# Optimization experiments

Measured on AMD Instinct MI355X. Metric: run time of the kernel, lower is better.

The kernel has to match this reference:

```python
import jax, jax.numpy as jnp
import numpy as np

N_ANCHORS = 262144
N_GT = 100
IMG = 1024.0
N_SAMPLE = 256
POS_RATIO = 0.5
POS_T = 0.7
NEG_T = 0.3
ALLOWED_BORDER = 0.0
NUM_FG = int(POS_RATIO * N_SAMPLE)  # 128


def compute_overlap(a, g):
    """IoU between anchors a:(N,4) and gt g:(R,4), py-faster-rcnn +1 pixel convention."""
    area_a = (a[:, 2] - a[:, 0] + 1.0) * (a[:, 3] - a[:, 1] + 1.0)          # (N,)
    area_g = (g[:, 2] - g[:, 0] + 1.0) * (g[:, 3] - g[:, 1] + 1.0)          # (R,)
    iw = jnp.minimum(a[:, None, 2], g[None, :, 2]) - jnp.maximum(a[:, None, 0], g[None, :, 0]) + 1.0
    ih = jnp.minimum(a[:, None, 3], g[None, :, 3]) - jnp.maximum(a[:, None, 1], g[None, :, 1]) + 1.0
    inter = jnp.maximum(iw, 0.0) * jnp.maximum(ih, 0.0)                     # (N,R)
    return inter / (area_a[:, None] + area_g[None, :] - inter)


def bbox_transform(gt, an):
    """Encode gt boxes relative to anchors -> (dx,dy,dw,dh), shape (N,4)."""
    aw = an[:, 2] - an[:, 0] + 1.0
    ah = an[:, 3] - an[:, 1] + 1.0
    acx = an[:, 0] + 0.5 * aw
    acy = an[:, 1] + 0.5 * ah
    gw = gt[:, 2] - gt[:, 0] + 1.0
    gh = gt[:, 3] - gt[:, 1] + 1.0
    gcx = gt[:, 0] + 0.5 * gw
    gcy = gt[:, 1] + 0.5 * gh
    return jnp.stack([(gcx - acx) / aw, (gcy - acy) / ah,
                      jnp.log(gw / aw), jnp.log(gh / ah)], axis=1)


def keep_at_most(mask, k, key):
    """Keep at most k True entries of mask, chosen uniformly at random (fixed shape)."""
    r = jnp.where(mask, jax.random.uniform(key, mask.shape), jnp.inf)
    rank = jnp.argsort(jnp.argsort(r))  # rank[i] = position of i in ascending sort
    return mask & (rank < k)


def anchor_target(anchors, image_shape, gt, key):
    # anchors: (N,4), gt: (R,4)
    R = gt.shape[0]
    inside = ((anchors[:, 0] >= -ALLOWED_BORDER) & (anchors[:, 1] >= -ALLOWED_BORDER)
              & (anchors[:, 2] < ALLOWED_BORDER + image_shape[1])
              & (anchors[:, 3] < ALLOWED_BORDER + image_shape[0]))            # (N,)
    iou = compute_overlap(anchors, gt)                                        # (N,R)
    iou_m = jnp.where(inside[:, None], iou, -1.0)  # restrict to inside anchors
    max_ov = jnp.max(iou_m, axis=1)                                           # (N,)

    k1, k2, k3 = jax.random.split(key, 3)
    labels = jnp.full(anchors.shape[:1], -1.0, dtype=jnp.float32)
    # clobber_positives=False: background first
    labels = jnp.where(inside & (max_ov < NEG_T), 0.0, labels)
    # per-gt argmax anchors (tie set), randomly truncated to at most R like tf.random_shuffle[:R]
    gt_max = jnp.max(iou_m, axis=0)                                           # (R,)
    cand = jnp.any(iou_m == gt_max[None, :], axis=1) & inside                 # (N,)
    cand = keep_at_most(cand, R, k1)
    labels = jnp.where(cand, 1.0, labels)
    labels = jnp.where(inside & (max_ov >= POS_T), 1.0, labels)

    # balance: subsample positives to NUM_FG
    fg = labels == 1.0
    labels = jnp.where(fg & ~keep_at_most(fg, NUM_FG, k2), -1.0, labels)
    # subsample negatives to n_sample - n_fg
    n_fg = jnp.sum(labels == 1.0)
    bg = labels == 0.0
    labels = jnp.where(bg & ~keep_at_most(bg, N_SAMPLE - n_fg, k3), -1.0, labels)
    # umap: outside anchors stay -1
    labels = jnp.where(inside, labels, -1.0)

    # bbox targets: faithful to original tf.gather(gt, to_int32(max_overlaps))
    idx = jnp.clip(max_ov.astype(jnp.int32), 0, R - 1)
    tgt = bbox_transform(gt[idx], anchors)                                    # (N,4)
    tgt = jnp.where(inside[:, None], tgt, 0.0)  # scatter_nd at inside indices
    return labels[None], tgt[None]


def setup_inputs() -> dict:
    key = jax.random.key(0)
    k1, k2, k3, k4 = jax.random.split(key, 4)
    ctr = jax.random.uniform(k1, (N_ANCHORS, 2), minval=-64.0, maxval=IMG + 64.0)
    wh = jax.random.uniform(k2, (N_ANCHORS, 2), minval=16.0, maxval=256.0)
    anchors = jnp.concatenate([ctr - 0.5 * wh, ctr + 0.5 * wh], axis=1)
    gctr = jax.random.uniform(k3, (N_GT, 2), minval=100.0, maxval=IMG - 100.0)
    gwh = jax.random.uniform(k4, (N_GT, 2), minval=30.0, maxval=200.0)
    gt = jnp.concatenate([gctr - 0.5 * gwh, gctr + 0.5 * gwh], axis=1)
    return {"total_anchors": anchors[None],
            "image_shape": jnp.array([IMG, IMG], jnp.float32),
            "gt_boxes": gt[None]}


def reference(total_anchors, image_shape, gt_boxes):
    key = jax.random.key(42)  # original uses unseeded tf.random_shuffle
    labels, bbox_reg_targets = anchor_target(total_anchors[0], image_shape,
                                             gt_boxes[0][:, :4], key)
    return labels, bbox_reg_targets
```

## Files before the change

### kernel.cpp

```cpp
#include <hip/hip_runtime.h>
#include <stdint.h>

#define NGT_MAX 128
#define CAND_CAP 8192
#define CSEL_CAP 512
#define FILT_CAP 16384
#define SUB_CAP 2048


__host__ __device__ inline void tf2x32(uint32_t k0, uint32_t k1, uint32_t c0, uint32_t c1,
                                       uint32_t& o0, uint32_t& o1) {
  uint32_t ks[3] = {k0, k1, k0 ^ k1 ^ 0x1BD11BDAu};
  uint32_t x0 = c0 + ks[0];
  uint32_t x1 = c1 + ks[1];
  const int rot[2][4] = {{13, 15, 26, 6}, {17, 29, 16, 24}};
#pragma unroll
  for (int i = 0; i < 5; ++i) {
#pragma unroll
    for (int j = 0; j < 4; ++j) {
      x0 += x1;
      int r = rot[i & 1][j];
      x1 = (x1 << r) | (x1 >> (32 - r));
      x1 ^= x0;
    }
    x0 += ks[(i + 1) % 3];
    x1 += ks[(i + 2) % 3] + (uint32_t)(i + 1);
  }
  o0 = x0; o1 = x1;
}

__device__ inline uint64_t sel_key(uint32_t i, uint32_t ka, uint32_t kb) {
  uint32_t o0, o1;
  tf2x32(ka, kb, 0u, i, o0, o1);
  uint32_t bits = o0 ^ o1;
  return ((uint64_t)(bits >> 9) << 32) | (uint64_t)i;
}

__device__ inline uint32_t fmap(float v) {
  uint32_t u = __float_as_uint(v);
  return (u & 0x80000000u) ? ~u : (u | 0x80000000u);
}
__device__ inline float funmap(uint32_t m) {
  return (m & 0x80000000u) ? __uint_as_float(m & 0x7FFFFFFFu) : __uint_as_float(~m);
}

__device__ inline void cons_meta(uint32_t baseF, uint32_t baseB, uint32_t* needF,
                                 uint32_t* Tf, uint32_t* needB, uint32_t* Tb) {
  *needF = (baseF > 128u) ? 1u : 0u;
  uint64_t tf = 0, tb = 0;
  if (*needF) {
    tf = (((uint64_t)(128u * 32u)) << 23) / (uint64_t)baseF;
    if (tf > (1u << 23)) tf = (1u << 23);
  }
  uint32_t nfgmin = baseF < 128u ? baseF : 128u;
  uint32_t kbgmax = 256u - nfgmin;
  *needB = (baseB > 8192u + kbgmax) ? 1u : 0u;
  if (*needB) {
    tb = (((uint64_t)(kbgmax * 32u)) << 23) / (uint64_t)(baseB - 8192u);
    if (tb > (1u << 23)) tb = (1u << 23);
  }
  *Tf = (uint32_t)tf;
  *Tb = (uint32_t)tb;
}

__device__ __forceinline__ float iou_ref(const float4& a, float area_a, const float4& gb,
                                         float area_g) {
#pragma clang fp contract(off)
  float iw = fminf(a.z, gb.z) - fmaxf(a.x, gb.x) + 1.0f;
  float ih = fminf(a.w, gb.w) - fmaxf(a.y, gb.y) + 1.0f;
  float inter = fmaxf(iw, 0.0f) * fmaxf(ih, 0.0f);
  return inter / (area_a + area_g - inter);
}

__device__ __forceinline__ float4 tgt_ref(const float4& a, const float4& gb) {
#pragma clang fp contract(off)
  float aw = a.z - a.x + 1.0f;
  float ah = a.w - a.y + 1.0f;
  float acx = a.x + 0.5f * aw;
  float acy = a.y + 0.5f * ah;
  float gw = gb.z - gb.x + 1.0f;
  float gh = gb.w - gb.y + 1.0f;
  float gcx = gb.x + 0.5f * gw;
  float gcy = gb.y + 0.5f * gh;
  return make_float4((gcx - acx) / aw, (gcy - acy) / ah, logf(gw / aw), logf(gh / ah));
}

__global__ void __launch_bounds__(256)
k_main(const float4* __restrict__ anc, const float* __restrict__ img,
       const float4* __restrict__ gt, int N, int R,
       uint32_t* __restrict__ pmax, uint32_t* __restrict__ gmaxu,
       float* __restrict__ LBL, float4* __restrict__ TGT,
       uint32_t* __restrict__ pmeta, uint32_t* __restrict__ counters) {
  __shared__ float4 sgt[NGT_MAX];
  __shared__ float sarea[NGT_MAX];
  __shared__ float sq[16 * 101];
  __shared__ uint32_t scnt[2];
  const int t = threadIdx.x, b = blockIdx.x;
  if (b == 0 && t < 16) counters[t] = 0u;
  if (t < 2) scnt[t] = 0u;
  if (t < R) {
    float4 g = gt[t];
    sgt[t] = g;
    {
#pragma clang fp contract(off)
      sarea[t] = (g.z - g.x + 1.0f) * (g.w - g.y + 1.0f);
    }
  }
  for (int j = t; j < 16 * 101; j += 256) sq[j] = -1.0f;
  __syncthreads();
  const int lane = t & 63, wid = t >> 6;
  const int h = lane >> 5;
  const int al = lane & 31;
  const int p = lane & 3;
  const int i = b * 128 + wid * 32 + al;
  const int gbase = 50 * h;
  const int Rh = R - gbase;
  const float H = img[0], W = img[1];
  float4 a = anc[i];
  bool inside = (a.x >= 0.0f) && (a.y >= 0.0f) && (a.z < W) && (a.w < H);
  float area_a;
  {
#pragma clang fp contract(off)
    area_a = (a.z - a.x + 1.0f) * (a.w - a.y + 1.0f);
  }
  if (!inside) area_a = __uint_as_float(0x7FC00000u);
  const bool b1 = (p == 1), b2 = (p == 2), b3 = (p == 3);
  float part[13];
  float vmax = -1.0f;
#pragma unroll
  for (int s = 0; s < 13; ++s) {
    float v2q[4];
#pragma unroll
    for (int k = 0; k < 4; ++k) {
      const int j = 4 * s + k;
      if (j < 50 && j < Rh) {
        const int g = gbase + j;
        float4 gb = sgt[g];
        float v = iou_ref(a, area_a, gb, sarea[g]);
        vmax = fmaxf(vmax, v);
        int d1 = __builtin_amdgcn_mov_dpp(__float_as_int(v), 0xB1, 0xF, 0xF, true);
        float v1 = fmaxf(v, __int_as_float(d1));
        int d2 = __builtin_amdgcn_mov_dpp(__float_as_int(v1), 0x4E, 0xF, 0xF, true);
        v2q[k] = fmaxf(v1, __int_as_float(d2));
      } else {
        v2q[k] = -1.0f;
      }
    }
    float pp = v2q[0];
    pp = b1 ? v2q[1] : pp;
    pp = b2 ? v2q[2] : pp;
    pp = b3 ? v2q[3] : pp;
    part[s] = pp;
  }
  vmax = fmaxf(vmax, __shfl_xor(vmax, 32));
  float lbl = -1.0f;
  if (inside) {
    if (vmax < 0.3f) lbl = 0.0f;
    if (vmax >= 0.7f) lbl = 1.0f;
  }
  unsigned long long bf = __ballot(lbl == 1.0f) & 0xFFFFFFFFull;
  unsigned long long bb = __ballot(lbl == 0.0f) & 0xFFFFFFFFull;
  if (lane == 0) {
    atomicAdd(&scnt[0], (uint32_t)__popcll(bf));
    atomicAdd(&scnt[1], (uint32_t)__popcll(bb));
  }
  if (h == 0) {
    LBL[i] = lbl;
    float4 o = make_float4(0.f, 0.f, 0.f, 0.f);
    if (inside) {
      int idx = (int)vmax;
      idx = idx < 0 ? 0 : (idx > R - 1 ? R - 1 : idx);
      o = tgt_ref(a, sgt[idx]);
    }
    TGT[i] = o;
  }
#pragma unroll
  for (int s = 0; s < 13; ++s) {
    float v = part[s];
    int x = __builtin_amdgcn_mov_dpp(__float_as_int(v), 0x114, 0xF, 0xF, true);
    v = fmaxf(v, __int_as_float(x));
    x = __builtin_amdgcn_mov_dpp(__float_as_int(v), 0x118, 0xF, 0xF, true);
    v = fmaxf(v, __int_as_float(x));
    part[s] = v;
  }
  const int r = t >> 4;
  if ((t & 15) >= 12) {
#pragma unroll
    for (int s = 0; s < 13; ++s) {
      const int j = 4 * s + p;
      if (j < 50 && j < Rh) sq[r * 101 + gbase + j] = part[s];
    }
  }
  __syncthreads();
  if (t < R) {
    float m = -1.0f;
#pragma unroll 8
    for (int r2 = 0; r2 < 16; ++r2) m = fmaxf(m, sq[r2 * 101 + t]);
    uint32_t u = fmap(m);
    pmax[b * R + t] = u;
    if (u > gmaxu[t]) atomicMax(&gmaxu[t], u);
  }
  if (t == 0) pmeta[b] = scnt[0] | (scnt[1] << 16);
}

__global__ void __launch_bounds__(256)
k_gather(const float4* __restrict__ anc, const float* __restrict__ img,
         const float4* __restrict__ gt, int N, int NBm, int R,
         const uint32_t* __restrict__ pmax, const uint32_t* __restrict__ gmaxu,
         const uint32_t* __restrict__ pmeta,
         float* __restrict__ LBL,
         uint64_t* __restrict__ candList, uint32_t* __restrict__ candLbl,
         uint64_t* __restrict__ listF, uint64_t* __restrict__ listB,
         uint32_t* __restrict__ counters,
         uint32_t k1a, uint32_t k1b, uint32_t k2a, uint32_t k2b,
         uint32_t k3a, uint32_t k3b) {
  __shared__ uint64_t red[256];
  __shared__ int tg[NGT_MAX];
  __shared__ float tgm[NGT_MAX];
  __shared__ uint64_t cbuf[256];
  __shared__ uint32_t cbufL[256];
  __shared__ uint64_t bufF[256], bufB[256];
  __shared__ uint32_t cC, cF, cB, oC, oF, oB;
  __shared__ int tcnt;
  const int t = threadIdx.x, b = blockIdx.x;
  if (t == 0) { tcnt = 0; cC = 0u; cF = 0u; cB = 0u; }
  uint64_t sm = 0;
  for (int j = t; j < NBm; j += 256) {
    uint32_t v = pmeta[j];
    sm += (uint64_t)(v & 0xFFFFu) | ((uint64_t)(v >> 16) << 32);
  }
  red[t] = sm;
  __syncthreads();
  for (int s = 128; s > 0; s >>= 1) {
    if (t < s) red[t] += red[t + s];
    __syncthreads();
  }
  const uint32_t baseF = (uint32_t)(red[0] & 0xFFFFFFFFu);
  const uint32_t baseB = (uint32_t)(red[0] >> 32);
  uint32_t needF, Tf, needB, Tb;
  cons_meta(baseF, baseB, &needF, &Tf, &needB, &Tb);
  if (t < R) {
    uint32_t gm = gmaxu[t];
    uint32_t pm0 = pmax[(2 * b) * R + t];
    uint32_t pm1 = pmax[(2 * b + 1) * R + t];
    if (pm0 == gm || pm1 == gm) {
      int pp = atomicAdd(&tcnt, 1);
      tg[pp] = t;
      tgm[pp] = funmap(gm);
    }
  }
  __syncthreads();
  const int C0 = tcnt;
  const int i = b * 256 + t;
  float old = LBL[i];
  bool isc = false;
  if (C0 > 0) {
    const float H = img[0], W = img[1];
    float4 a = anc[i];
    bool inside = (a.x >= 0.0f) && (a.y >= 0.0f) && (a.z < W) && (a.w < H);
    if (inside) {
      float area_a;
      {
#pragma clang fp contract(off)
        area_a = (a.z - a.x + 1.0f) * (a.w - a.y + 1.0f);
      }
      for (int j = 0; j < C0; ++j) {
        float4 gb = gt[tg[j]];
        float ag;
        {
#pragma clang fp contract(off)
          ag = (gb.z - gb.x + 1.0f) * (gb.w - gb.y + 1.0f);
        }
        float v = iou_ref(a, area_a, gb, ag);
        isc = isc || (v == tgm[j]);
      }
    }
  }
  if (isc) {
    uint32_t code = (old == 1.0f) ? 2u : ((old == 0.0f) ? 1u : 0u);
    uint32_t pp = atomicAdd(&cC, 1u);
    cbuf[pp] = sel_key((uint32_t)i, k1a, k1b);
    cbufL[pp] = code;
  }
  float l1 = isc ? 1.0f : old;
  float out = l1;
  if (l1 == 1.0f) {
    uint64_t key = sel_key((uint32_t)i, k2a, k2b);
    if (needF && (uint32_t)(key >> 32) >= Tf) {
      out = -1.0f;
    } else {
      uint32_t pp = atomicAdd(&cF, 1u);
      bufF[pp] = key;
    }
  } else if (l1 == 0.0f) {
    uint64_t key = sel_key((uint32_t)i, k3a, k3b);
    if (needB && (uint32_t)(key >> 32) >= Tb) {
      out = -1.0f;
    } else {
      uint32_t pp = atomicAdd(&cB, 1u);
      bufB[pp] = key;
    }
  }
  LBL[i] = out;
  __syncthreads();
  if (t == 0 && cC) oC = atomicAdd(&counters[0], cC);
  if (t == 64 && cF) oF = atomicAdd(&counters[4], cF);
  if (t == 128 && cB) oB = atomicAdd(&counters[5], cB);
  __syncthreads();
  for (uint32_t j = t; j < cC; j += 256) {
    uint32_t pp = oC + j;
    if (pp < CAND_CAP) { candList[pp] = cbuf[j]; candLbl[pp] = cbufL[j]; }
  }
  for (uint32_t j = t; j < cF; j += 256) {
    uint32_t pp = oF + j;
    if (pp < FILT_CAP) listF[pp] = bufF[j];
  }
  for (uint32_t j = t; j < cB; j += 256) {
    uint32_t pp = oB + j;
    if (pp < FILT_CAP) listB[pp] = bufB[j];
  }
}

__device__ __forceinline__ void do_select(const uint64_t* list, uint32_t Mf, uint32_t k,
                                          uint32_t T, float* LBL, uint32_t* h,
                                          uint32_t* c0, uint32_t* c1, uint64_t* sub,
                                          uint32_t* scal, const uint32_t* drop,
                                          uint32_t nd) {
  const int t = threadIdx.x;
  if (Mf <= k) return;
  int bl = (T > 1u) ? (32 - __clz(T - 1u)) : 0;
  int shift = bl > 8 ? bl - 8 : 0;
  h[t] = 0u;
  if (t == 0) { scal[0] = 0u; scal[1] = 0u; scal[2] = 0u; }
  __syncthreads();
  for (uint32_t j = t; j < Mf; j += 256) {
    uint64_t key = list[j];
    bool skip = false;
    for (uint32_t d = 0; d < nd; ++d) skip = skip || (drop[d] == (uint32_t)key);
    if (!skip) atomicAdd(&h[((uint32_t)(key >> 32)) >> shift], 1u);
  }
  __syncthreads();
  c0[t] = h[t];
  __syncthreads();
  uint32_t* s = c0;
  uint32_t* d2 = c1;
  for (int dd = 1; dd < 256; dd <<= 1) {
    uint32_t v = s[t];
    if (t >= dd) v += s[t - dd];
    d2[t] = v;
    __syncthreads();
    uint32_t* tmp = s; s = d2; d2 = tmp;
  }
  uint32_t inc = s[t];
  uint32_t exc = inc - h[t];
  if (exc < k && inc >= k) { scal[1] = (uint32_t)t; scal[2] = k - exc; }
  __syncthreads();
  const uint32_t binb = scal[1], rneed = scal[2];
  for (uint32_t j = t; j < Mf; j += 256) {
    uint64_t key = list[j];
    bool skip = false;
    for (uint32_t d = 0; d < nd; ++d) skip = skip || (drop[d] == (uint32_t)key);
    if (skip) continue;
    uint32_t bin = ((uint32_t)(key >> 32)) >> shift;
    if (bin > binb) {
      LBL[(uint32_t)key] = -1.0f;
    } else if (bin == binb) {
      uint32_t pp = atomicAdd(&scal[0], 1u);
      if (pp < SUB_CAP) sub[pp] = key;
    }
  }
  __syncthreads();
  uint32_t c = scal[0] < SUB_CAP ? scal[0] : SUB_CAP;
  for (uint32_t s2 = t; s2 < c; s2 += 256) {
    uint64_t key = sub[s2];
    uint32_t rank = 0u;
    for (uint32_t j = 0; j < c; ++j) rank += (sub[j] < key) ? 1u : 0u;
    if (rank >= rneed) LBL[(uint32_t)key] = -1.0f;
  }
  __syncthreads();
}

__global__ void __launch_bounds__(256)
k_sel(float* __restrict__ LBL, uint64_t* __restrict__ listF,
      uint64_t* __restrict__ listB, const uint64_t* __restrict__ candList,
      const uint32_t* __restrict__ candLbl, const uint32_t* __restrict__ pmeta,
      uint32_t* __restrict__ counters, int NBm, int R,
      uint32_t k3a, uint32_t k3b) {
  __shared__ uint64_t red[256];
  __shared__ uint64_t ck[CSEL_CAP];
  __shared__ uint32_t cc[CSEL_CAP];
  __shared__ uint32_t drop[256];
  __shared__ uint32_t h[256], c0s[256], c1s[256];
  __shared__ uint64_t sub[SUB_CAP];
  __shared__ uint32_t scal[8];
  const int t = threadIdx.x;
  uint64_t sm = 0;
  for (int j = t; j < NBm; j += 256) {
    uint32_t v = pmeta[j];
    sm += (uint64_t)(v & 0xFFFFu) | ((uint64_t)(v >> 16) << 32);
  }
  red[t] = sm;
  if (t < 8) scal[t] = 0u;
  uint32_t C = counters[0];
  if (C > CSEL_CAP) C = CSEL_CAP;
  for (uint32_t s = t; s < C; s += 256) { ck[s] = candList[s]; cc[s] = candLbl[s]; }
  __syncthreads();
  for (int s = 128; s > 0; s >>= 1) {
    if (t < s) red[t] += red[t + s];
    __syncthreads();
  }
  const uint32_t baseF = (uint32_t)(red[0] & 0xFFFFFFFFu);
  const uint32_t baseB = (uint32_t)(red[0] >> 32);
  uint32_t needFc, TfC, needBc, TbC;
  cons_meta(baseF, baseB, &needFc, &TfC, &needBc, &TbC);
  const uint32_t MfB0 = counters[5] < FILT_CAP ? counters[5] : FILT_CAP;
  for (uint32_t e = t; e < C; e += 256) {
    uint64_t key = ck[e];
    bool keep = true;
    if (C > (uint32_t)R) {
      uint32_t rank = 0;
      for (uint32_t j = 0; j < C; ++j) rank += (ck[j] < key) ? 1u : 0u;
      keep = (rank < (uint32_t)R);
    }
    uint32_t code = cc[e];
    uint32_t idx = (uint32_t)key;
    if (keep) {
      if (code != 2u) atomicAdd(&scal[4], 1u);
      if (code == 1u) atomicAdd(&scal[5], 1u);
    } else if (code != 2u) {
      uint32_t pp = atomicAdd(&scal[3], 1u);
      if (pp < 256) drop[pp] = idx;
      if (code == 0u) {
        LBL[idx] = -1.0f;
      } else {
        uint64_t key3 = sel_key(idx, k3a, k3b);
        if (needBc && (uint32_t)(key3 >> 32) >= TbC) {
          LBL[idx] = -1.0f;
        } else {
          uint32_t qq = atomicAdd(&scal[6], 1u);
          if (MfB0 + qq < FILT_CAP) listB[MfB0 + qq] = key3;
          LBL[idx] = 0.0f;
        }
      }
    }
  }
  __syncthreads();
  const uint32_t fgflips = scal[4], bgflips = scal[5];
  const uint32_t nDrop = scal[3] < 256u ? scal[3] : 256u;
  const uint32_t nAdd = scal[6];
  const uint32_t M1 = baseF + fgflips;
  const uint32_t M2 = baseB - bgflips;
  const uint32_t nfg = M1 < 128u ? M1 : 128u;
  const uint32_t kbg = 256u - nfg;
  if (M1 > 128u) {
    uint32_t MfF = counters[4] < FILT_CAP ? counters[4] : FILT_CAP;
    uint32_t TF = needFc ? TfC : (1u << 23);
    do_select(listF, MfF, 128u, TF, LBL, h, c0s, c1s, sub, scal, drop, nDrop);
  }
  if (M2 > kbg) {
    uint32_t MfB = MfB0 + nAdd;
    if (MfB > FILT_CAP) MfB = FILT_CAP;
    uint32_t TB = needBc ? TbC : (1u << 23);
    do_select(listB, MfB, kbg, TB, LBL, h, c0s, c1s, sub, scal, drop, 0u);
  }
}

extern "C" void kernel_launch(void* const* d_in, const int* in_sizes, int n_in,
                              void* d_out, int out_size, void* d_ws, size_t ws_size,
                              hipStream_t stream) {
  (void)n_in; (void)out_size; (void)ws_size;
  const int N = in_sizes[0] / 4;
  const int R = in_sizes[2] / 4;
  const int NBm = N / 128;
  const int NBg = N / 256;
  const float4* anc = (const float4*)d_in[0];
  const float* img = (const float*)d_in[1];
  const float4* gtb = (const float4*)d_in[2];
  float* LBL = (float*)d_out;
  float4* TGT = (float4*)((float*)d_out + N);

  uint8_t* ws = (uint8_t*)d_ws;
  uint32_t* counters = (uint32_t*)ws;
  uint32_t* gmaxu = (uint32_t*)(ws + 512);
  uint32_t* pmeta = (uint32_t*)(ws + 1024);
  uint32_t* candLbl = (uint32_t*)(ws + 16384);
  uint32_t* pmax = (uint32_t*)(ws + 65536);
  size_t off = 65536 + (size_t)NBm * R * 4;
  off = (off + 7) & ~(size_t)7;
  uint64_t* candList = (uint64_t*)(ws + off);
  uint64_t* listF = (uint64_t*)(ws + off + CAND_CAP * 8);
  uint64_t* listB = (uint64_t*)(ws + off + CAND_CAP * 8 + FILT_CAP * 8);

  uint32_t k1a, k1b, k2a, k2b, k3a, k3b;
  tf2x32(0u, 42u, 0u, 0u, k1a, k1b);
  tf2x32(0u, 42u, 0u, 1u, k2a, k2b);
  tf2x32(0u, 42u, 0u, 2u, k3a, k3b);

  k_main<<<NBm, 256, 0, stream>>>(anc, img, gtb, N, R, pmax, gmaxu, LBL, TGT, pmeta,
                                  counters);
  k_gather<<<NBg, 256, 0, stream>>>(anc, img, gtb, N, NBm, R, pmax, gmaxu, pmeta, LBL,
                                    candList, candLbl, listF, listB, counters,
                                    k1a, k1b, k2a, k2b, k3a, k3b);
  k_sel<<<1, 256, 0, stream>>>(LBL, listF, listB, candList, candLbl, pmeta, counters,
                               NBm, R, k3a, k3b);
}
```

Before: 136.6 us.

## Fuse gather and select kernels via last-block ticket, replace pmeta reduction with atomics

```diff
diff --git a/kernel.cpp b/kernel.cpp
--- a/kernel.cpp
+++ b/kernel.cpp
@@ -90,13 +90,12 @@
        const float4* __restrict__ gt, int N, int R,
        uint32_t* __restrict__ pmax, uint32_t* __restrict__ gmaxu,
        float* __restrict__ LBL, float4* __restrict__ TGT,
-       uint32_t* __restrict__ pmeta, uint32_t* __restrict__ counters) {
+       uint32_t* __restrict__ counters) {
   __shared__ float4 sgt[NGT_MAX];
   __shared__ float sarea[NGT_MAX];
   __shared__ float sq[16 * 101];
   __shared__ uint32_t scnt[2];
   const int t = threadIdx.x, b = blockIdx.x;
-  if (b == 0 && t < 16) counters[t] = 0u;
   if (t < 2) scnt[t] = 0u;
   if (t < R) {
     float4 g = gt[t];
@@ -200,126 +199,30 @@
     pmax[b * R + t] = u;
     if (u > gmaxu[t]) atomicMax(&gmaxu[t], u);
   }
-  if (t == 0) pmeta[b] = scnt[0] | (scnt[1] << 16);
-}
-
-__global__ void __launch_bounds__(256)
-k_gather(const float4* __restrict__ anc, const float* __restrict__ img,
-         const float4* __restrict__ gt, int N, int NBm, int R,
-         const uint32_t* __restrict__ pmax, const uint32_t* __restrict__ gmaxu,
-         const uint32_t* __restrict__ pmeta,
-         float* __restrict__ LBL,
-         uint64_t* __restrict__ candList, uint32_t* __restrict__ candLbl,
-         uint64_t* __restrict__ listF, uint64_t* __restrict__ listB,
-         uint32_t* __restrict__ counters,
-         uint32_t k1a, uint32_t k1b, uint32_t k2a, uint32_t k2b,
-         uint32_t k3a, uint32_t k3b) {
-  __shared__ uint64_t red[256];
-  __shared__ int tg[NGT_MAX];
-  __shared__ float tgm[NGT_MAX];
-  __shared__ uint64_t cbuf[256];
-  __shared__ uint32_t cbufL[256];
-  __shared__ uint64_t bufF[256], bufB[256];
-  __shared__ uint32_t cC, cF, cB, oC, oF, oB;
-  __shared__ int tcnt;
-  const int t = threadIdx.x, b = blockIdx.x;
-  if (t == 0) { tcnt = 0; cC = 0u; cF = 0u; cB = 0u; }
-  uint64_t sm = 0;
-  for (int j = t; j < NBm; j += 256) {
-    uint32_t v = pmeta[j];
-    sm += (uint64_t)(v & 0xFFFFu) | ((uint64_t)(v >> 16) << 32);
-  }
-  red[t] = sm;
-  __syncthreads();
-  for (int s = 128; s > 0; s >>= 1) {
-    if (t < s) red[t] += red[t + s];
-    __syncthreads();
-  }
-  const uint32_t baseF = (uint32_t)(red[0] & 0xFFFFFFFFu);
-  const uint32_t baseB = (uint32_t)(red[0] >> 32);
-  uint32_t needF, Tf, needB, Tb;
-  cons_meta(baseF, baseB, &needF, &Tf, &needB, &Tb);
-  if (t < R) {
-    uint32_t gm = gmaxu[t];
-    uint32_t pm0 = pmax[(2 * b) * R + t];
-    uint32_t pm1 = pmax[(2 * b + 1) * R + t];
-    if (pm0 == gm || pm1 == gm) {
-      int pp = atomicAdd(&tcnt, 1);
-      tg[pp] = t;
-      tgm[pp] = funmap(gm);
-    }
-  }
-  __syncthreads();
-  const int C0 = tcnt;
-  const int i = b * 256 + t;
-  float old = LBL[i];
-  bool isc = false;
-  if (C0 > 0) {
-    const float H = img[0], W = img[1];
-    float4 a = anc[i];
-    bool inside = (a.x >= 0.0f) && (a.y >= 0.0f) && (a.z < W) && (a.w < H);
-    if (inside) {
-      float area_a;
-      {
-#pragma clang fp contract(off)
-        area_a = (a.z - a.x + 1.0f) * (a.w - a.y + 1.0f);
-      }
-      for (int j = 0; j < C0; ++j) {
-        float4 gb = gt[tg[j]];
-        float ag;
-        {
-#pragma clang fp contract(off)
-          ag = (gb.z - gb.x + 1.0f) * (gb.w - gb.y + 1.0f);
-        }
-        float v = iou_ref(a, area_a, gb, ag);
-        isc = isc || (v == tgm[j]);
-      }
-    }
-  }
-  if (isc) {
-    uint32_t code = (old == 1.0f) ? 2u : ((old == 0.0f) ? 1u : 0u);
-    uint32_t pp = atomicAdd(&cC, 1u);
-    cbuf[pp] = sel_key((uint32_t)i, k1a, k1b);
-    cbufL[pp] = code;
-  }
-  float l1 = isc ? 1.0f : old;
-  float out = l1;
-  if (l1 == 1.0f) {
-    uint64_t key = sel_key((uint32_t)i, k2a, k2b);
-    if (needF && (uint32_t)(key >> 32) >= Tf) {
-      out = -1.0f;
-    } else {
-      uint32_t pp = atomicAdd(&cF, 1u);
-      bufF[pp] = key;
-    }
-  } else if (l1 == 0.0f) {
-    uint64_t key = sel_key((uint32_t)i, k3a, k3b);
-    if (needB && (uint32_t)(key >> 32) >= Tb) {
-      out = -1.0f;
-    } else {
-      uint32_t pp = atomicAdd(&cB, 1u);
-      bufB[pp] = key;
-    }
-  }
-  LBL[i] = out;
-  __syncthreads();
-  if (t == 0 && cC) oC = atomicAdd(&counters[0], cC);
-  if (t == 64 && cF) oF = atomicAdd(&counters[4], cF);
-  if (t == 128 && cB) oB = atomicAdd(&counters[5], cB);
-  __syncthreads();
-  for (uint32_t j = t; j < cC; j += 256) {
-    uint32_t pp = oC + j;
-    if (pp < CAND_CAP) { candList[pp] = cbuf[j]; candLbl[pp] = cbufL[j]; }
-  }
-  for (uint32_t j = t; j < cF; j += 256) {
-    uint32_t pp = oF + j;
-    if (pp < FILT_CAP) listF[pp] = bufF[j];
-  }
-  for (uint32_t j = t; j < cB; j += 256) {
-    uint32_t pp = oB + j;
-    if (pp < FILT_CAP) listB[pp] = bufB[j];
-  }
-}
+  if (t == 0) {
+    atomicAdd(&counters[8], scnt[0]);
+    atomicAdd(&counters[9], scnt[1]);
+  }
+}
+
+struct GPart {
+  uint64_t cbuf[256];
+  uint64_t bufF[256];
+  uint64_t bufB[256];
+  uint32_t cbufL[256];
+  int tg[NGT_MAX];
+  float tgm[NGT_MAX];
+};
+struct SPart {
+  uint64_t ck[CSEL_CAP];
+  uint64_t sub[SUB_CAP];
+  uint32_t cc[CSEL_CAP];
+  uint32_t drop[256];
+  uint32_t hist[256];
+  uint32_t c0s[256];
+  uint32_t c1s[256];
+};
+union GSU { GPart g; SPart s; };
 
 __device__ __forceinline__ void do_select(const uint64_t* list, uint32_t Mf, uint32_t k,
                                           uint32_t T, float* LBL, uint32_t* h,
@@ -381,60 +284,152 @@
 }
 
 __global__ void __launch_bounds__(256)
-k_sel(float* __restrict__ LBL, uint64_t* __restrict__ listF,
-      uint64_t* __restrict__ listB, const uint64_t* __restrict__ candList,
-      const uint32_t* __restrict__ candLbl, const uint32_t* __restrict__ pmeta,
-      uint32_t* __restrict__ counters, int NBm, int R,
-      uint32_t k3a, uint32_t k3b) {
-  __shared__ uint64_t red[256];
-  __shared__ uint64_t ck[CSEL_CAP];
-  __shared__ uint32_t cc[CSEL_CAP];
-  __shared__ uint32_t drop[256];
-  __shared__ uint32_t h[256], c0s[256], c1s[256];
-  __shared__ uint64_t sub[SUB_CAP];
+k_gsel(const float4* __restrict__ anc, const float* __restrict__ img,
+       const float4* __restrict__ gt, int N, int R,
+       const uint32_t* __restrict__ pmax, const uint32_t* __restrict__ gmaxu,
+       float* __restrict__ LBL,
+       uint64_t* __restrict__ candList, uint32_t* __restrict__ candLbl,
+       uint64_t* __restrict__ listF, uint64_t* __restrict__ listB,
+       uint32_t* __restrict__ counters,
+       uint32_t k1a, uint32_t k1b, uint32_t k2a, uint32_t k2b,
+       uint32_t k3a, uint32_t k3b) {
+  __shared__ GSU u;
+  __shared__ float4 sgt[NGT_MAX];
+  __shared__ float sarea[NGT_MAX];
+  __shared__ uint32_t sbase[2];
   __shared__ uint32_t scal[8];
-  const int t = threadIdx.x;
-  uint64_t sm = 0;
-  for (int j = t; j < NBm; j += 256) {
-    uint32_t v = pmeta[j];
-    sm += (uint64_t)(v & 0xFFFFu) | ((uint64_t)(v >> 16) << 32);
-  }
-  red[t] = sm;
+  __shared__ int tcnt;
+  __shared__ uint32_t cC, cF, cB, oC, oF, oB, sticket;
+  const int t = threadIdx.x, b = blockIdx.x;
+  const int NBg = gridDim.x;
+  if (t == 0) {
+    tcnt = 0; cC = 0u; cF = 0u; cB = 0u;
+    sbase[0] = counters[8];
+    sbase[1] = counters[9];
+  }
+  if (t < R) {
+    float4 g = gt[t];
+    sgt[t] = g;
+    {
+#pragma clang fp contract(off)
+      sarea[t] = (g.z - g.x + 1.0f) * (g.w - g.y + 1.0f);
+    }
+  }
+  __syncthreads();
+  const uint32_t baseF = sbase[0];
+  const uint32_t baseB = sbase[1];
+  uint32_t needF, Tf, needB, Tb;
+  cons_meta(baseF, baseB, &needF, &Tf, &needB, &Tb);
+  if (t < R) {
+    uint32_t gm = gmaxu[t];
+    uint32_t pm0 = pmax[(2 * b) * R + t];
+    uint32_t pm1 = pmax[(2 * b + 1) * R + t];
+    if (pm0 == gm || pm1 == gm) {
+      int pp = atomicAdd(&tcnt, 1);
+      u.g.tg[pp] = t;
+      u.g.tgm[pp] = funmap(gm);
+    }
+  }
+  __syncthreads();
+  const int C0 = tcnt;
+  const int i = b * 256 + t;
+  const float H = img[0], W = img[1];
+  float old = LBL[i];
+  bool isc = false;
+  if (C0 > 0) {
+    float4 a = anc[i];
+    bool inside = (a.x >= 0.0f) && (a.y >= 0.0f) && (a.z < W) && (a.w < H);
+    if (inside) {
+      float area_a;
+      {
+#pragma clang fp contract(off)
+        area_a = (a.z - a.x + 1.0f) * (a.w - a.y + 1.0f);
+      }
+      for (int j = 0; j < C0; ++j) {
+        int g = u.g.tg[j];
+        float v = iou_ref(a, area_a, sgt[g], sarea[g]);
+        isc = isc || (v == u.g.tgm[j]);
+      }
+    }
+  }
+  if (isc) {
+    uint32_t code = (old == 1.0f) ? 2u : ((old == 0.0f) ? 1u : 0u);
+    uint32_t pp = atomicAdd(&cC, 1u);
+    u.g.cbuf[pp] = sel_key((uint32_t)i, k1a, k1b);
+    u.g.cbufL[pp] = code;
+  }
+  float l1 = isc ? 1.0f : old;
+  float out = l1;
+  if (l1 == 1.0f) {
+    uint64_t key = sel_key((uint32_t)i, k2a, k2b);
+    if (needF && (uint32_t)(key >> 32) >= Tf) {
+      out = -1.0f;
+    } else {
+      uint32_t pp = atomicAdd(&cF, 1u);
+      u.g.bufF[pp] = key;
+    }
+  } else if (l1 == 0.0f) {
+    uint64_t key = sel_key((uint32_t)i, k3a, k3b);
+    if (needB && (uint32_t)(key >> 32) >= Tb) {
+      out = -1.0f;
+    } else {
+      uint32_t pp = atomicAdd(&cB, 1u);
+      u.g.bufB[pp] = key;
+    }
+  }
+  LBL[i] = out;
+  __syncthreads();
+  if (t == 0 && cC) oC = atomicAdd(&counters[0], cC);
+  if (t == 64 && cF) oF = atomicAdd(&counters[4], cF);
+  if (t == 128 && cB) oB = atomicAdd(&counters[5], cB);
+  __syncthreads();
+  for (uint32_t j = t; j < cC; j += 256) {
+    uint32_t pp = oC + j;
+    if (pp < CAND_CAP) { candList[pp] = u.g.cbuf[j]; candLbl[pp] = u.g.cbufL[j]; }
+  }
+  for (uint32_t j = t; j < cF; j += 256) {
+    uint32_t pp = oF + j;
+    if (pp < FILT_CAP) listF[pp] = u.g.bufF[j];
+  }
+  for (uint32_t j = t; j < cB; j += 256) {
+    uint32_t pp = oB + j;
+    if (pp < FILT_CAP) listB[pp] = u.g.bufB[j];
+  }
+  __threadfence();
+  __syncthreads();
+  if (t == 0) sticket = atomicAdd(&counters[3], 1u);
+  __syncthreads();
+  if (sticket != (uint32_t)(NBg - 1)) return;
+  __threadfence();
+
   if (t < 8) scal[t] = 0u;
-  uint32_t C = counters[0];
+  uint32_t C = atomicAdd(&counters[0], 0u);
   if (C > CSEL_CAP) C = CSEL_CAP;
-  for (uint32_t s = t; s < C; s += 256) { ck[s] = candList[s]; cc[s] = candLbl[s]; }
-  __syncthreads();
-  for (int s = 128; s > 0; s >>= 1) {
-    if (t < s) red[t] += red[t + s];
-    __syncthreads();
-  }
-  const uint32_t baseF = (uint32_t)(red[0] & 0xFFFFFFFFu);
-  const uint32_t baseB = (uint32_t)(red[0] >> 32);
-  uint32_t needFc, TfC, needBc, TbC;
-  cons_meta(baseF, baseB, &needFc, &TfC, &needBc, &TbC);
-  const uint32_t MfB0 = counters[5] < FILT_CAP ? counters[5] : FILT_CAP;
+  for (uint32_t s = t; s < C; s += 256) { u.s.ck[s] = candList[s]; u.s.cc[s] = candLbl[s]; }
+  __syncthreads();
+  const uint32_t MfB0raw = atomicAdd(&counters[5], 0u);
+  const uint32_t MfB0 = MfB0raw < FILT_CAP ? MfB0raw : FILT_CAP;
   for (uint32_t e = t; e < C; e += 256) {
-    uint64_t key = ck[e];
+    uint64_t key = u.s.ck[e];
     bool keep = true;
     if (C > (uint32_t)R) {
       uint32_t rank = 0;
-      for (uint32_t j = 0; j < C; ++j) rank += (ck[j] < key) ? 1u : 0u;
+      for (uint32_t j = 0; j < C; ++j) rank += (u.s.ck[j] < key) ? 1u : 0u;
       keep = (rank < (uint32_t)R);
     }
-    uint32_t code = cc[e];
+    uint32_t code = u.s.cc[e];
     uint32_t idx = (uint32_t)key;
     if (keep) {
       if (code != 2u) atomicAdd(&scal[4], 1u);
       if (code == 1u) atomicAdd(&scal[5], 1u);
     } else if (code != 2u) {
       uint32_t pp = atomicAdd(&scal[3], 1u);
-      if (pp < 256) drop[pp] = idx;
+      if (pp < 256) u.s.drop[pp] = idx;
       if (code == 0u) {
         LBL[idx] = -1.0f;
       } else {
         uint64_t key3 = sel_key(idx, k3a, k3b);
-        if (needBc && (uint32_t)(key3 >> 32) >= TbC) {
+        if (needB && (uint32_t)(key3 >> 32) >= Tb) {
           LBL[idx] = -1.0f;
         } else {
           uint32_t qq = atomicAdd(&scal[6], 1u);
@@ -453,15 +448,18 @@
   const uint32_t nfg = M1 < 128u ? M1 : 128u;
   const uint32_t kbg = 256u - nfg;
   if (M1 > 128u) {
-    uint32_t MfF = counters[4] < FILT_CAP ? counters[4] : FILT_CAP;
-    uint32_t TF = needFc ? TfC : (1u << 23);
-    do_select(listF, MfF, 128u, TF, LBL, h, c0s, c1s, sub, scal, drop, nDrop);
+    uint32_t MfFraw = atomicAdd(&counters[4], 0u);
+    uint32_t MfF = MfFraw < FILT_CAP ? MfFraw : FILT_CAP;
+    uint32_t TF = needF ? Tf : (1u << 23);
+    do_select(listF, MfF, 128u, TF, LBL, u.s.hist, u.s.c0s, u.s.c1s, u.s.sub, scal,
+              u.s.drop, nDrop);
   }
   if (M2 > kbg) {
     uint32_t MfB = MfB0 + nAdd;
     if (MfB > FILT_CAP) MfB = FILT_CAP;
-    uint32_t TB = needBc ? TbC : (1u << 23);
-    do_select(listB, MfB, kbg, TB, LBL, h, c0s, c1s, sub, scal, drop, 0u);
+    uint32_t TB = needB ? Tb : (1u << 23);
+    do_select(listB, MfB, kbg, TB, LBL, u.s.hist, u.s.c0s, u.s.c1s, u.s.sub, scal,
+              u.s.drop, 0u);
   }
 }
 
@@ -482,7 +480,6 @@
   uint8_t* ws = (uint8_t*)d_ws;
   uint32_t* counters = (uint32_t*)ws;
   uint32_t* gmaxu = (uint32_t*)(ws + 512);
-  uint32_t* pmeta = (uint32_t*)(ws + 1024);
   uint32_t* candLbl = (uint32_t*)(ws + 16384);
   uint32_t* pmax = (uint32_t*)(ws + 65536);
   size_t off = 65536 + (size_t)NBm * R * 4;
@@ -496,11 +493,10 @@
   tf2x32(0u, 42u, 0u, 1u, k2a, k2b);
   tf2x32(0u, 42u, 0u, 2u, k3a, k3b);
 
-  k_main<<<NBm, 256, 0, stream>>>(anc, img, gtb, N, R, pmax, gmaxu, LBL, TGT, pmeta,
+  hipMemsetAsync(counters, 0, 64, stream);
+  k_main<<<NBm, 256, 0, stream>>>(anc, img, gtb, N, R, pmax, gmaxu, LBL, TGT,
                                   counters);
-  k_gather<<<NBg, 256, 0, stream>>>(anc, img, gtb, N, NBm, R, pmax, gmaxu, pmeta, LBL,
-                                    candList, candLbl, listF, listB, counters,
-                                    k1a, k1b, k2a, k2b, k3a, k3b);
-  k_sel<<<1, 256, 0, stream>>>(LBL, listF, listB, candList, candLbl, pmeta, counters,
-                               NBm, R, k3a, k3b);
-}
+  k_gsel<<<NBg, 256, 0, stream>>>(anc, img, gtb, N, R, pmax, gmaxu, LBL,
+                                  candList, candLbl, listF, listB, counters,
+                                  k1a, k1b, k2a, k2b, k3a, k3b);
+}
```

Result: slower. 215.2 us (+57.5%).
